# Kernel tuning notes

Hardware: AMD Instinct MI355X
Metric: run time of the kernel (lower is better)

## Reference

```python
import jax, jax.numpy as jnp
import numpy as np

B, L, DIM = 4, 9216, 256
NH, NP = 8, 4
HD = DIM // NH  # 32
SIDE = int(np.sqrt(L))  # 96


def setup_inputs() -> dict:
    key = jax.random.key(0)
    ks = jax.random.split(key, 8)
    s = 0.05
    return {
        "query": jax.random.normal(ks[0], (B, L, DIM), jnp.float32),
        "key": jax.random.normal(ks[1], (B, L, DIM), jnp.float32),
        "value": jax.random.normal(ks[2], (B, L, DIM), jnp.float32),
        "Wv": jax.random.normal(ks[3], (DIM, DIM), jnp.float32) * s,
        "bv": jnp.zeros((DIM,), jnp.float32),
        "Woff": jax.random.normal(ks[4], (DIM, NH * NP * 2), jnp.float32) * s,
        "boff": jnp.zeros((NH * NP * 2,), jnp.float32),
        "Wwt": jax.random.normal(ks[5], (DIM, NH * NP), jnp.float32) * s,
        "bwt": jnp.zeros((NH * NP,), jnp.float32),
        "Wo": jax.random.normal(ks[6], (DIM, DIM), jnp.float32) * s,
        "bo": jnp.zeros((DIM,), jnp.float32),
    }


def _deform_attn(query, value, Wv, bv, Woff, boff, Wwt, bwt, Wo, bo):
    Bq, Lq, D = query.shape
    h = w = SIDE
    # value projection -> [B, nH, L, hd]
    v = (value @ Wv + bv).reshape(Bq, Lq, NH, HD).transpose(0, 2, 1, 3)
    # reference points in [0,1]: ref[...,0]=x (varies fast), ref[...,1]=y (row-major flatten)
    ys = jnp.linspace(0.0, 1.0, h)
    xs = jnp.linspace(0.0, 1.0, w)
    y_ref = jnp.repeat(ys, w)  # [L]
    x_ref = jnp.tile(xs, h)    # [L]
    ref = jnp.stack([x_ref, y_ref], axis=-1)  # [L, 2]
    # offsets [B, nH, Lq, NP, 2] and softmax weights [B, nH, Lq, NP]
    offset = (query @ Woff + boff).reshape(Bq, Lq, NH, NP, 2).transpose(0, 2, 1, 3, 4)
    wt = jax.nn.softmax(
        (query @ Wwt + bwt).reshape(Bq, Lq, NH, NP).transpose(0, 2, 1, 3), axis=-1
    )
    loc = jnp.clip(ref[None, None, :, None, :] + offset, 0.0, 1.0)
    # faithful to source: component 0 scales by (h-1) -> row, component 1 by (w-1) -> col
    rows = loc[..., 0] * (h - 1)  # [B, nH, Lq, NP]
    cols = loc[..., 1] * (w - 1)
    r0 = jnp.floor(rows)
    c0 = jnp.floor(cols)
    fr = (rows - r0)[..., None]  # [B, nH, Lq, NP, 1]
    fc = (cols - c0)[..., None]
    r0i = r0.astype(jnp.int32)
    c0i = c0.astype(jnp.int32)
    r1i = jnp.minimum(r0i + 1, h - 1)
    c1i = jnp.minimum(c0i + 1, w - 1)

    def gather(ri, ci):
        idx = (ri * w + ci).reshape(Bq, NH, Lq * NP)
        g = jnp.take_along_axis(v, idx[..., None], axis=2)  # [B, nH, Lq*NP, hd]
        return g.reshape(Bq, NH, Lq, NP, HD)

    samp = (
        gather(r0i, c0i) * (1.0 - fr) * (1.0 - fc)
        + gather(r0i, c1i) * (1.0 - fr) * fc
        + gather(r1i, c0i) * fr * (1.0 - fc)
        + gather(r1i, c1i) * fr * fc
    )  # [B, nH, Lq, NP, hd]
    out = jnp.einsum("bhqp,bhqpd->bhqd", wt, samp)
    out = out.transpose(0, 2, 1, 3).reshape(Bq, Lq, D)
    return out @ Wo + bo


def reference(query, key, value, Wv, bv, Woff, boff, Wwt, bwt, Wo, bo):
    # key never influences the output in the source module (k is computed but unused)
    return _deform_attn(query, value, Wv, bv, Woff, boff, Wwt, bwt, Wo, bo)
```

## Files before the change

kernel.cpp:

```cpp
#include <hip/hip_runtime.h>
#include <hip/hip_bf16.h>

#define Bq   4
#define Lq   9216
#define DIMc 256
#define NHc  8
#define NPc  4
#define HDc  32
#define SIDEc 96

using f32x4  = __attribute__((ext_vector_type(4))) float;
using bf16x8 = __attribute__((ext_vector_type(8))) short;
using u16x8  = __attribute__((ext_vector_type(8))) unsigned short;

static __device__ __forceinline__ short f2bf(float x) {
    union { __hip_bfloat16 h; short s; } u;
    u.h = __float2bfloat16(x);
    return u.s;
}
static __device__ __forceinline__ float bfbits(unsigned short s) {
    union { unsigned u; float f; } v; v.u = ((unsigned)s) << 16; return v.f;
}

__global__ void prep(const float* __restrict__ Wv, const float* __restrict__ Wo,
                     const float* __restrict__ Woff, const float* __restrict__ Wwt,
                     short* __restrict__ WvT, short* __restrict__ WoT,
                     short* __restrict__ WpHi, short* __restrict__ WpLo) {
    const int id = blockIdx.x, t = threadIdx.x;
    if (id < 64) {
        __shared__ float tile[256][8];
        const float* W = (id < 32) ? Wv : Wo;
        short* T = (id < 32) ? WvT : WoT;
        const int n0 = (id & 31) * 8;
        const float4 a = *(const float4*)&W[t * 256 + n0];
        const float4 b = *(const float4*)&W[t * 256 + n0 + 4];
        tile[t][0] = a.x; tile[t][1] = a.y; tile[t][2] = a.z; tile[t][3] = a.w;
        tile[t][4] = b.x; tile[t][5] = b.y; tile[t][6] = b.z; tile[t][7] = b.w;
        __syncthreads();
        const int n = n0 + (t >> 5), kk = (t & 31) * 8;
        bf16x8 v;
#pragma unroll
        for (int e = 0; e < 8; ++e) v[e] = f2bf(tile[kk + e][t >> 5]);
        *(bf16x8*)&T[n * 256 + kk] = v;
    } else {
        const int p = id - 64;
        const float x = (p < 64) ? Woff[t * 64 + p] : Wwt[t * 32 + (p - 64)];
        const short h = f2bf(x);
        WpHi[p * 256 + t] = h;
        WpLo[p * 256 + t] = f2bf(x - bfbits((unsigned short)h));
    }
}

template<bool VOUT, bool BF16IN>
__global__ __launch_bounds__(256, 3) void gemm_mfma(
        const float* __restrict__ Xf, const short* Xb,
        const short* __restrict__ WT, const float* __restrict__ bias,
        __hip_bfloat16* __restrict__ Yv, float* Yo) {
    __shared__ short As[64][264];
    const int t = threadIdx.x;
    const int base = blockIdx.x * 64;

    if (BF16IN) {
#pragma unroll
        for (int p = 0; p < 8; ++p) {
            const int c = p * 256 + t;
            const int r = c >> 5, k0 = (c & 31) * 8;
            *(bf16x8*)&As[r][k0] = *(const bf16x8*)&Xb[((long)blockIdx.x << 15) + r * 256 + k0];
        }
    } else {
        const float4* X4 = (const float4*)(Xf + (long)base * DIMc);
#pragma unroll
        for (int p = 0; p < 8; ++p) {
            const int c = p * 256 + t;
            const int r = c >> 5, kq = (c & 31) * 2;
            const float4 a = X4[r * 64 + kq];
            const float4 b = X4[r * 64 + kq + 1];
            bf16x8 v;
            v[0] = f2bf(a.x); v[1] = f2bf(a.y); v[2] = f2bf(a.z); v[3] = f2bf(a.w);
            v[4] = f2bf(b.x); v[5] = f2bf(b.y); v[6] = f2bf(b.z); v[7] = f2bf(b.w);
            *(bf16x8*)&As[r][kq * 4] = v;
        }
    }
    __syncthreads();

    const int lane = t & 63, wc = t >> 6;
    const int lr = lane & 15, lq = lane >> 4;

    f32x4 acc[4][4];
#pragma unroll
    for (int i = 0; i < 4; ++i)
#pragma unroll
        for (int j = 0; j < 4; ++j) acc[i][j] = (f32x4){0.f, 0.f, 0.f, 0.f};

#pragma unroll
    for (int ks = 0; ks < 8; ++ks) {
        const int k0 = ks * 32 + lq * 8;
        bf16x8 a[4], b[4];
#pragma unroll
        for (int i = 0; i < 4; ++i)
            a[i] = *(const bf16x8*)&As[i * 16 + lr][k0];
#pragma unroll
        for (int j = 0; j < 4; ++j)
            b[j] = *(const bf16x8*)&WT[(wc * 64 + j * 16 + lr) * 256 + k0];
#pragma unroll
        for (int i = 0; i < 4; ++i)
#pragma unroll
            for (int j = 0; j < 4; ++j)
                acc[i][j] = __builtin_amdgcn_mfma_f32_16x16x32_bf16(a[i], b[j], acc[i][j], 0, 0, 0);
    }

    const int b_ = base / Lq;
    const int l0 = base % Lq;
#pragma unroll
    for (int i = 0; i < 4; ++i) {
        const int mrow = i * 16 + lq * 4;
#pragma unroll
        for (int j = 0; j < 4; ++j) {
            const int n  = wc * 64 + j * 16 + lr;
            const float bb = bias[n];
            const f32x4 v = acc[i][j];
            if (VOUT) {
                const int h = n >> 5, d = n & 31;
                __hip_bfloat16* yb = Yv + (((long)(b_ * NHc + h)) * Lq + (l0 + mrow)) * HDc + d;
#pragma unroll
                for (int reg = 0; reg < 4; ++reg)
                    yb[(long)reg * HDc] = __float2bfloat16(v[reg] + bb);
            } else {
                float* yo = Yo + (long)(base + mrow) * DIMc + n;
#pragma unroll
                for (int reg = 0; reg < 4; ++reg)
                    yo[(long)reg * DIMc] = v[reg] + bb;
            }
        }
    }
}

__global__ __launch_bounds__(256, 3) void deform_fused2(
        const float* __restrict__ Q,
        const short* __restrict__ WpHi, const short* __restrict__ WpLo,
        const float* __restrict__ boff, const float* __restrict__ bwt,
        const __hip_bfloat16* __restrict__ vws,
        __hip_bfloat16* __restrict__ midb) {
    __shared__ float  Qf[32][260];
    __shared__ int    recI[1024];
    __shared__ float4 recW[1024];
    float* prjs = &Qf[0][0];

    const int t = threadIdx.x;
    const int bid = (int)blockIdx.x;
    const int lb = (bid & 7) * 144 + (bid >> 3);
    const int base = lb * 32;
    const int b  = base / Lq;
    const int l0 = base % Lq;

    const float4* Q4 = (const float4*)(Q + (long)base * DIMc);
#pragma unroll
    for (int p = 0; p < 8; ++p) {
        const int c = p * 256 + t;
        const int r = c >> 6, kq = c & 63;
        *(float4*)&Qf[r][kq * 4] = Q4[c];
    }
    __syncthreads();

    const int lane = t & 63, w = t >> 6;
    const int rt = w & 1, cg = w >> 1;
    const int lr = lane & 15, lq = lane >> 4;

    f32x4 pacc[3];
#pragma unroll
    for (int jj = 0; jj < 3; ++jj) pacc[jj] = (f32x4){0.f, 0.f, 0.f, 0.f};

#pragma unroll
    for (int ks = 0; ks < 8; ++ks) {
        const int k0 = ks * 32 + lq * 8;
        const float* qp = &Qf[rt * 16 + lr][k0];
        const float4 a0 = *(const float4*)qp;
        const float4 a1 = *(const float4*)(qp + 4);
        const float xs[8] = {a0.x, a0.y, a0.z, a0.w, a1.x, a1.y, a1.z, a1.w};
        bf16x8 ah, al;
#pragma unroll
        for (int e = 0; e < 8; ++e) {
            const short hh = f2bf(xs[e]);
            ah[e] = hh;
            al[e] = f2bf(xs[e] - bfbits((unsigned short)hh));
        }
#pragma unroll
        for (int jj = 0; jj < 3; ++jj) {
            const int c = cg * 48 + jj * 16 + lr;
            const bf16x8 bh = *(const bf16x8*)&WpHi[c * 256 + k0];
            const bf16x8 bl = *(const bf16x8*)&WpLo[c * 256 + k0];
            pacc[jj] = __builtin_amdgcn_mfma_f32_16x16x32_bf16(ah, bh, pacc[jj], 0, 0, 0);
            pacc[jj] = __builtin_amdgcn_mfma_f32_16x16x32_bf16(ah, bl, pacc[jj], 0, 0, 0);
            pacc[jj] = __builtin_amdgcn_mfma_f32_16x16x32_bf16(al, bh, pacc[jj], 0, 0, 0);
        }
    }
    __syncthreads();

#pragma unroll
    for (int jj = 0; jj < 3; ++jj) {
        const int col = cg * 48 + jj * 16 + lr;
        const float bb = (col < 64) ? boff[col] : bwt[col - 64];
#pragma unroll
        for (int reg = 0; reg < 4; ++reg) {
            const int row = rt * 16 + lq * 4 + reg;
            prjs[row * 96 + col] = pacc[jj][reg] + bb;
        }
    }
    __syncthreads();

#pragma unroll
    for (int i = 0; i < 4; ++i) {
        const int s = i * 256 + t;
        const int r = s >> 5, u = s & 31;
        const int h = u >> 2, p = u & 3;
        const int l = l0 + r;
        const float* pr = &prjs[r * 96];
        const float inv = 1.0f / (SIDEc - 1);
        const float xr = (float)(l % SIDEc) * inv;
        const float yr = (float)(l / SIDEc) * inv;

        const float4 lg = *(const float4*)&pr[64 + h * 4];
        const float m = fmaxf(fmaxf(lg.x, lg.y), fmaxf(lg.z, lg.w));
        const float e0 = expf(lg.x - m), e1 = expf(lg.y - m);
        const float e2 = expf(lg.z - m), e3 = expf(lg.w - m);
        const float sum = e0 + e1 + e2 + e3;
        const float ep = (p == 0) ? e0 : (p == 1) ? e1 : (p == 2) ? e2 : e3;
        const float wt = ep / sum;

        const float lx = fminf(fmaxf(xr + pr[u * 2 + 0], 0.f), 1.f);
        const float ly = fminf(fmaxf(yr + pr[u * 2 + 1], 0.f), 1.f);
        const float rowf = lx * (float)(SIDEc - 1);
        const float colf = ly * (float)(SIDEc - 1);
        const float r0f = floorf(rowf), c0f = floorf(colf);
        const int r0 = (int)r0f, c0 = (int)c0f;
        const float fr = rowf - r0f, fc = colf - c0f;
        const int drow = (r0 < SIDEc - 1) ? 1 : 0;
        const int dcol = (c0 < SIDEc - 1) ? 1 : 0;
        recI[s] = (r0 * SIDEc + c0) | (drow << 16) | (dcol << 17);
        float4 w4;
        w4.x = wt * (1.f - fr) * (1.f - fc);
        w4.y = wt * (1.f - fr) * fc;
        w4.z = wt * fr * (1.f - fc);
        w4.w = wt * fr * fc;
        recW[s] = w4;
    }
    __syncthreads();

    const int h = (t >> 2) & 7, dq = t & 3;
    const int rhalf = (t >> 5) & 1, wid = t >> 6;
    const __hip_bfloat16* vb = vws + ((long)(b * NHc + h) * Lq) * HDc + dq * 8;
    const int chan = (t & 31) * 8;

#pragma unroll
    for (int pass = 0; pass < 4; ++pass) {
        const int r = pass * 8 + wid * 2 + rhalf;
        float acc[8];
#pragma unroll
        for (int e = 0; e < 8; ++e) acc[e] = 0.f;
#pragma unroll
        for (int p = 0; p < 4; ++p) {
            const int    mt = recI[r * 32 + h * 4 + p];
            const float4 w4 = recW[r * 32 + h * 4 + p];
            const int sl = mt & 0xFFFF;
            const int dr = (mt & 0x10000) ? SIDEc * HDc : 0;
            const int dc = (mt & 0x20000) ? HDc : 0;
            const __hip_bfloat16* pv = vb + (long)sl * HDc;
            const u16x8 u00 = *(const u16x8*)(pv);
            const u16x8 u01 = *(const u16x8*)(pv + dc);
            const u16x8 u10 = *(const u16x8*)(pv + dr);
            const u16x8 u11 = *(const u16x8*)(pv + dr + dc);
#pragma unroll
            for (int e = 0; e < 8; ++e)
                acc[e] += w4.x * bfbits(u00[e]) + w4.y * bfbits(u01[e])
                        + w4.z * bfbits(u10[e]) + w4.w * bfbits(u11[e]);
        }
        const int rg = base + r;
        u16x8 o;
#pragma unroll
        for (int e = 0; e < 8; ++e) o[e] = (unsigned short)f2bf(acc[e]);
        *(u16x8*)(midb + ((long)(rg >> 6) << 15) + ((rg & 63) << 8) + chan) = o;
    }
}

extern "C" void kernel_launch(void* const* d_in, const int* in_sizes, int n_in,
                              void* d_out, int out_size, void* d_ws, size_t ws_size,
                              hipStream_t stream) {
    const float* query = (const float*)d_in[0];
    const float* value = (const float*)d_in[2];
    const float* Wv    = (const float*)d_in[3];
    const float* bv    = (const float*)d_in[4];
    const float* Woff  = (const float*)d_in[5];
    const float* boff  = (const float*)d_in[6];
    const float* Wwt   = (const float*)d_in[7];
    const float* bwt   = (const float*)d_in[8];
    const float* Wo    = (const float*)d_in[9];
    const float* bo    = (const float*)d_in[10];

    float* out = (float*)d_out;
    char*  ws  = (char*)d_ws;
    __hip_bfloat16* vws = (__hip_bfloat16*)ws;
    short* WvT  = (short*)(ws + 18874368);
    short* WoT  = (short*)(ws + 18874368 + 131072);
    short* WpHi = (short*)(ws + 18874368 + 262144);
    short* WpLo = (short*)(ws + 18874368 + 262144 + 49152);
    __hip_bfloat16* midb = (__hip_bfloat16*)d_out;

    const int nrows = Bq * Lq;

    prep<<<160, 256, 0, stream>>>(Wv, Wo, Woff, Wwt, WvT, WoT, WpHi, WpLo);
    gemm_mfma<true, false><<<nrows / 64, 256, 0, stream>>>(value, nullptr, WvT, bv, vws, nullptr);
    deform_fused2<<<nrows / 32, 256, 0, stream>>>(query, WpHi, WpLo, boff, bwt, vws, midb);
    gemm_mfma<false, true><<<nrows / 64, 256, 0, stream>>>(nullptr, (const short*)midb, WoT, bo, nullptr, out);
}
```

Measured before the change: 100.2 us.

## Move offset/weight projection into value GEMM kernel, slim gather kernel

Moves the query projection (offsets and softmax logits, split bf16 hi/lo MFMA) out of the deform kernel and into the value-projection GEMM kernel, which now writes fp32 projections to a workspace buffer. The gather kernel only loads the 96-wide projections, so its LDS footprint shrinks and it can run at higher occupancy (launch bounds 6). Bilinear weights are now stored as fp16 in LDS, which costs a little precision. Both GEMMs now use 32-row tiles instead of 64, which doubles the block count. The price is an extra global round trip for the projection buffer.

```diff
diff --git a/kernel.cpp b/kernel.cpp
--- a/kernel.cpp
+++ b/kernel.cpp
@@ -12,6 +12,7 @@
 using f32x4  = __attribute__((ext_vector_type(4))) float;
 using bf16x8 = __attribute__((ext_vector_type(8))) short;
 using u16x8  = __attribute__((ext_vector_type(8))) unsigned short;
+using h16x4  = __attribute__((ext_vector_type(4))) _Float16;
 
 static __device__ __forceinline__ short f2bf(float x) {
     union { __hip_bfloat16 h; short s; } u;
@@ -51,59 +52,93 @@
     }
 }
 
-template<bool VOUT, bool BF16IN>
-__global__ __launch_bounds__(256, 3) void gemm_mfma(
-        const float* __restrict__ Xf, const short* Xb,
-        const short* __restrict__ WT, const float* __restrict__ bias,
-        __hip_bfloat16* __restrict__ Yv, float* Yo) {
-    __shared__ short As[64][264];
+__global__ __launch_bounds__(256, 3) void gemm1_proj(
+        const float* __restrict__ X, const float* __restrict__ Q,
+        const short* __restrict__ WT,
+        const short* __restrict__ WpHi, const short* __restrict__ WpLo,
+        const float* __restrict__ bias,
+        const float* __restrict__ boff, const float* __restrict__ bwt,
+        __hip_bfloat16* __restrict__ Yv, float* __restrict__ prj) {
+    __shared__ short As[32][264];
     const int t = threadIdx.x;
-    const int base = blockIdx.x * 64;
-
-    if (BF16IN) {
-#pragma unroll
-        for (int p = 0; p < 8; ++p) {
-            const int c = p * 256 + t;
-            const int r = c >> 5, k0 = (c & 31) * 8;
-            *(bf16x8*)&As[r][k0] = *(const bf16x8*)&Xb[((long)blockIdx.x << 15) + r * 256 + k0];
-        }
-    } else {
-        const float4* X4 = (const float4*)(Xf + (long)base * DIMc);
-#pragma unroll
-        for (int p = 0; p < 8; ++p) {
-            const int c = p * 256 + t;
-            const int r = c >> 5, kq = (c & 31) * 2;
-            const float4 a = X4[r * 64 + kq];
-            const float4 b = X4[r * 64 + kq + 1];
-            bf16x8 v;
-            v[0] = f2bf(a.x); v[1] = f2bf(a.y); v[2] = f2bf(a.z); v[3] = f2bf(a.w);
-            v[4] = f2bf(b.x); v[5] = f2bf(b.y); v[6] = f2bf(b.z); v[7] = f2bf(b.w);
-            *(bf16x8*)&As[r][kq * 4] = v;
+    const int base = blockIdx.x * 32;
+
+    const float4* X4 = (const float4*)(X + (long)base * DIMc);
+#pragma unroll
+    for (int p = 0; p < 4; ++p) {
+        const int c = p * 256 + t;
+        const int r = c >> 5, kq = (c & 31) * 2;
+        const float4 a = X4[r * 64 + kq];
+        const float4 b = X4[r * 64 + kq + 1];
+        bf16x8 v;
+        v[0] = f2bf(a.x); v[1] = f2bf(a.y); v[2] = f2bf(a.z); v[3] = f2bf(a.w);
+        v[4] = f2bf(b.x); v[5] = f2bf(b.y); v[6] = f2bf(b.z); v[7] = f2bf(b.w);
+        *(bf16x8*)&As[r][kq * 4] = v;
+    }
+
+    const int lane = t & 63, w = t >> 6;
+    const int lr = lane & 15, lq = lane >> 4;
+
+    {
+        const int rt = w >> 1, cg = w & 1;
+        f32x4 pacc[3];
+#pragma unroll
+        for (int jj = 0; jj < 3; ++jj) pacc[jj] = (f32x4){0.f, 0.f, 0.f, 0.f};
+        const float* Qrow = Q + (long)(base + rt * 16 + lr) * DIMc;
+#pragma unroll
+        for (int ks = 0; ks < 8; ++ks) {
+            const int k0 = ks * 32 + lq * 8;
+            const float4 a0 = *(const float4*)(Qrow + k0);
+            const float4 a1 = *(const float4*)(Qrow + k0 + 4);
+            const float xs[8] = {a0.x, a0.y, a0.z, a0.w, a1.x, a1.y, a1.z, a1.w};
+            bf16x8 ah, al;
+#pragma unroll
+            for (int e = 0; e < 8; ++e) {
+                const short hh = f2bf(xs[e]);
+                ah[e] = hh;
+                al[e] = f2bf(xs[e] - bfbits((unsigned short)hh));
+            }
+#pragma unroll
+            for (int jj = 0; jj < 3; ++jj) {
+                const int c = cg * 48 + jj * 16 + lr;
+                const bf16x8 bh = *(const bf16x8*)&WpHi[c * 256 + k0];
+                const bf16x8 bl = *(const bf16x8*)&WpLo[c * 256 + k0];
+                pacc[jj] = __builtin_amdgcn_mfma_f32_16x16x32_bf16(ah, bh, pacc[jj], 0, 0, 0);
+                pacc[jj] = __builtin_amdgcn_mfma_f32_16x16x32_bf16(ah, bl, pacc[jj], 0, 0, 0);
+                pacc[jj] = __builtin_amdgcn_mfma_f32_16x16x32_bf16(al, bh, pacc[jj], 0, 0, 0);
+            }
+        }
+#pragma unroll
+        for (int jj = 0; jj < 3; ++jj) {
+            const int col = cg * 48 + jj * 16 + lr;
+            const float bb = (col < 64) ? boff[col] : bwt[col - 64];
+#pragma unroll
+            for (int reg = 0; reg < 4; ++reg) {
+                const int row = rt * 16 + lq * 4 + reg;
+                prj[(long)(base + row) * 96 + col] = pacc[jj][reg] + bb;
+            }
         }
     }
     __syncthreads();
 
-    const int lane = t & 63, wc = t >> 6;
-    const int lr = lane & 15, lq = lane >> 4;
-
-    f32x4 acc[4][4];
-#pragma unroll
-    for (int i = 0; i < 4; ++i)
+    f32x4 acc[2][4];
+#pragma unroll
+    for (int i = 0; i < 2; ++i)
 #pragma unroll
         for (int j = 0; j < 4; ++j) acc[i][j] = (f32x4){0.f, 0.f, 0.f, 0.f};
 
 #pragma unroll
     for (int ks = 0; ks < 8; ++ks) {
         const int k0 = ks * 32 + lq * 8;
-        bf16x8 a[4], b[4];
-#pragma unroll
-        for (int i = 0; i < 4; ++i)
+        bf16x8 a[2], b[4];
+#pragma unroll
+        for (int i = 0; i < 2; ++i)
             a[i] = *(const bf16x8*)&As[i * 16 + lr][k0];
 #pragma unroll
         for (int j = 0; j < 4; ++j)
-            b[j] = *(const bf16x8*)&WT[(wc * 64 + j * 16 + lr) * 256 + k0];
-#pragma unroll
-        for (int i = 0; i < 4; ++i)
+            b[j] = *(const bf16x8*)&WT[(w * 64 + j * 16 + lr) * 256 + k0];
+#pragma unroll
+        for (int i = 0; i < 2; ++i)
 #pragma unroll
             for (int j = 0; j < 4; ++j)
                 acc[i][j] = __builtin_amdgcn_mfma_f32_16x16x32_bf16(a[i], b[j], acc[i][j], 0, 0, 0);
@@ -112,39 +147,29 @@
     const int b_ = base / Lq;
     const int l0 = base % Lq;
 #pragma unroll
-    for (int i = 0; i < 4; ++i) {
+    for (int i = 0; i < 2; ++i) {
         const int mrow = i * 16 + lq * 4;
 #pragma unroll
         for (int j = 0; j < 4; ++j) {
-            const int n  = wc * 64 + j * 16 + lr;
+            const int n  = w * 64 + j * 16 + lr;
             const float bb = bias[n];
             const f32x4 v = acc[i][j];
-            if (VOUT) {
-                const int h = n >> 5, d = n & 31;
-                __hip_bfloat16* yb = Yv + (((long)(b_ * NHc + h)) * Lq + (l0 + mrow)) * HDc + d;
-#pragma unroll
-                for (int reg = 0; reg < 4; ++reg)
-                    yb[(long)reg * HDc] = __float2bfloat16(v[reg] + bb);
-            } else {
-                float* yo = Yo + (long)(base + mrow) * DIMc + n;
-#pragma unroll
-                for (int reg = 0; reg < 4; ++reg)
-                    yo[(long)reg * DIMc] = v[reg] + bb;
-            }
-        }
-    }
-}
-
-__global__ __launch_bounds__(256, 3) void deform_fused2(
-        const float* __restrict__ Q,
-        const short* __restrict__ WpHi, const short* __restrict__ WpLo,
-        const float* __restrict__ boff, const float* __restrict__ bwt,
+            const int h = n >> 5, d = n & 31;
+            __hip_bfloat16* yb = Yv + (((long)(b_ * NHc + h)) * Lq + (l0 + mrow)) * HDc + d;
+#pragma unroll
+            for (int reg = 0; reg < 4; ++reg)
+                yb[(long)reg * HDc] = __float2bfloat16(v[reg] + bb);
+        }
+    }
+}
+
+__global__ __launch_bounds__(256, 6) void deform_gather(
+        const float* __restrict__ prj,
         const __hip_bfloat16* __restrict__ vws,
         __hip_bfloat16* __restrict__ midb) {
-    __shared__ float  Qf[32][260];
-    __shared__ int    recI[1024];
-    __shared__ float4 recW[1024];
-    float* prjs = &Qf[0][0];
+    __shared__ float prjs[32 * 96];
+    __shared__ int   recI[1024];
+    __shared__ h16x4 recW[1024];
 
     const int t = threadIdx.x;
     const int bid = (int)blockIdx.x;
@@ -153,59 +178,10 @@
     const int b  = base / Lq;
     const int l0 = base % Lq;
 
-    const float4* Q4 = (const float4*)(Q + (long)base * DIMc);
-#pragma unroll
-    for (int p = 0; p < 8; ++p) {
-        const int c = p * 256 + t;
-        const int r = c >> 6, kq = c & 63;
-        *(float4*)&Qf[r][kq * 4] = Q4[c];
-    }
-    __syncthreads();
-
-    const int lane = t & 63, w = t >> 6;
-    const int rt = w & 1, cg = w >> 1;
-    const int lr = lane & 15, lq = lane >> 4;
-
-    f32x4 pacc[3];
-#pragma unroll
-    for (int jj = 0; jj < 3; ++jj) pacc[jj] = (f32x4){0.f, 0.f, 0.f, 0.f};
-
-#pragma unroll
-    for (int ks = 0; ks < 8; ++ks) {
-        const int k0 = ks * 32 + lq * 8;
-        const float* qp = &Qf[rt * 16 + lr][k0];
-        const float4 a0 = *(const float4*)qp;
-        const float4 a1 = *(const float4*)(qp + 4);
-        const float xs[8] = {a0.x, a0.y, a0.z, a0.w, a1.x, a1.y, a1.z, a1.w};
-        bf16x8 ah, al;
-#pragma unroll
-        for (int e = 0; e < 8; ++e) {
-            const short hh = f2bf(xs[e]);
-            ah[e] = hh;
-            al[e] = f2bf(xs[e] - bfbits((unsigned short)hh));
-        }
-#pragma unroll
-        for (int jj = 0; jj < 3; ++jj) {
-            const int c = cg * 48 + jj * 16 + lr;
-            const bf16x8 bh = *(const bf16x8*)&WpHi[c * 256 + k0];
-            const bf16x8 bl = *(const bf16x8*)&WpLo[c * 256 + k0];
-            pacc[jj] = __builtin_amdgcn_mfma_f32_16x16x32_bf16(ah, bh, pacc[jj], 0, 0, 0);
-            pacc[jj] = __builtin_amdgcn_mfma_f32_16x16x32_bf16(ah, bl, pacc[jj], 0, 0, 0);
-            pacc[jj] = __builtin_amdgcn_mfma_f32_16x16x32_bf16(al, bh, pacc[jj], 0, 0, 0);
-        }
-    }
-    __syncthreads();
-
-#pragma unroll
-    for (int jj = 0; jj < 3; ++jj) {
-        const int col = cg * 48 + jj * 16 + lr;
-        const float bb = (col < 64) ? boff[col] : bwt[col - 64];
-#pragma unroll
-        for (int reg = 0; reg < 4; ++reg) {
-            const int row = rt * 16 + lq * 4 + reg;
-            prjs[row * 96 + col] = pacc[jj][reg] + bb;
-        }
-    }
+    const float4* P4 = (const float4*)(prj + (long)base * 96);
+#pragma unroll
+    for (int i = 0; i < 3; ++i)
+        ((float4*)prjs)[t + 256 * i] = P4[t + 256 * i];
     __syncthreads();
 
 #pragma unroll
@@ -237,12 +213,12 @@
         const int drow = (r0 < SIDEc - 1) ? 1 : 0;
         const int dcol = (c0 < SIDEc - 1) ? 1 : 0;
         recI[s] = (r0 * SIDEc + c0) | (drow << 16) | (dcol << 17);
-        float4 w4;
-        w4.x = wt * (1.f - fr) * (1.f - fc);
-        w4.y = wt * (1.f - fr) * fc;
-        w4.z = wt * fr * (1.f - fc);
-        w4.w = wt * fr * fc;
-        recW[s] = w4;
+        h16x4 wh;
+        wh[0] = (_Float16)(wt * (1.f - fr) * (1.f - fc));
+        wh[1] = (_Float16)(wt * (1.f - fr) * fc);
+        wh[2] = (_Float16)(wt * fr * (1.f - fc));
+        wh[3] = (_Float16)(wt * fr * fc);
+        recW[s] = wh;
     }
     __syncthreads();
 
@@ -259,8 +235,10 @@
         for (int e = 0; e < 8; ++e) acc[e] = 0.f;
 #pragma unroll
         for (int p = 0; p < 4; ++p) {
-            const int    mt = recI[r * 32 + h * 4 + p];
-            const float4 w4 = recW[r * 32 + h * 4 + p];
+            const int   mt = recI[r * 32 + h * 4 + p];
+            const h16x4 wh = recW[r * 32 + h * 4 + p];
+            const float w0 = (float)wh[0], w1 = (float)wh[1];
+            const float w2 = (float)wh[2], w3 = (float)wh[3];
             const int sl = mt & 0xFFFF;
             const int dr = (mt & 0x10000) ? SIDEc * HDc : 0;
             const int dc = (mt & 0x20000) ? HDc : 0;
@@ -271,14 +249,71 @@
             const u16x8 u11 = *(const u16x8*)(pv + dr + dc);
 #pragma unroll
             for (int e = 0; e < 8; ++e)
-                acc[e] += w4.x * bfbits(u00[e]) + w4.y * bfbits(u01[e])
-                        + w4.z * bfbits(u10[e]) + w4.w * bfbits(u11[e]);
+                acc[e] += w0 * bfbits(u00[e]) + w1 * bfbits(u01[e])
+                        + w2 * bfbits(u10[e]) + w3 * bfbits(u11[e]);
         }
         const int rg = base + r;
         u16x8 o;
 #pragma unroll
         for (int e = 0; e < 8; ++e) o[e] = (unsigned short)f2bf(acc[e]);
-        *(u16x8*)(midb + ((long)(rg >> 6) << 15) + ((rg & 63) << 8) + chan) = o;
+        *(u16x8*)(midb + ((long)(rg >> 5) << 14) + ((rg & 31) << 8) + chan) = o;
+    }
+}
+
+__global__ __launch_bounds__(256, 4) void gemm2_mfma(
+        const short* Xb, const short* __restrict__ WT,
+        const float* __restrict__ bias, float* Yo) {
+    __shared__ short As[32][264];
+    const int t = threadIdx.x;
+    const int base = blockIdx.x * 32;
+
+#pragma unroll
+    for (int p = 0; p < 4; ++p) {
+        const int c = p * 256 + t;
+        const int r = c >> 5, k0 = (c & 31) * 8;
+        *(bf16x8*)&As[r][k0] = *(const bf16x8*)&Xb[((long)blockIdx.x << 14) + r * 256 + k0];
+    }
+    __syncthreads();
+
+    const int lane = t & 63, w = t >> 6;
+    const int lr = lane & 15, lq = lane >> 4;
+
+    f32x4 acc[2][4];
+#pragma unroll
+    for (int i = 0; i < 2; ++i)
+#pragma unroll
+        for (int j = 0; j < 4; ++j) acc[i][j] = (f32x4){0.f, 0.f, 0.f, 0.f};
+
+#pragma unroll
+    for (int ks = 0; ks < 8; ++ks) {
+        const int k0 = ks * 32 + lq * 8;
+        bf16x8 a[2], b[4];
+#pragma unroll
+        for (int i = 0; i < 2; ++i)
+            a[i] = *(const bf16x8*)&As[i * 16 + lr][k0];
+#pragma unroll
+        for (int j = 0; j < 4; ++j)
+            b[j] = *(const bf16x8*)&WT[(w * 64 + j * 16 + lr) * 256 + k0];
+#pragma unroll
+        for (int i = 0; i < 2; ++i)
+#pragma unroll
+            for (int j = 0; j < 4; ++j)
+                acc[i][j] = __builtin_amdgcn_mfma_f32_16x16x32_bf16(a[i], b[j], acc[i][j], 0, 0, 0);
+    }
+
+#pragma unroll
+    for (int i = 0; i < 2; ++i) {
+        const int mrow = i * 16 + lq * 4;
+#pragma unroll
+        for (int j = 0; j < 4; ++j) {
+            const int n  = w * 64 + j * 16 + lr;
+            const float bb = bias[n];
+            const f32x4 v = acc[i][j];
+            float* yo = Yo + (long)(base + mrow) * DIMc + n;
+#pragma unroll
+            for (int reg = 0; reg < 4; ++reg)
+                yo[(long)reg * DIMc] = v[reg] + bb;
+        }
     }
 }
 
@@ -303,12 +338,14 @@
     short* WoT  = (short*)(ws + 18874368 + 131072);
     short* WpHi = (short*)(ws + 18874368 + 262144);
     short* WpLo = (short*)(ws + 18874368 + 262144 + 49152);
+    float* prj  = (float*)(ws + 18874368 + 262144 + 98304);
     __hip_bfloat16* midb = (__hip_bfloat16*)d_out;
 
     const int nrows = Bq * Lq;
 
     prep<<<160, 256, 0, stream>>>(Wv, Wo, Woff, Wwt, WvT, WoT, WpHi, WpLo);
-    gemm_mfma<true, false><<<nrows / 64, 256, 0, stream>>>(value, nullptr, WvT, bv, vws, nullptr);
-    deform_fused2<<<nrows / 32, 256, 0, stream>>>(query, WpHi, WpLo, boff, bwt, vws, midb);
-    gemm_mfma<false, true><<<nrows / 64, 256, 0, stream>>>(nullptr, (const short*)midb, WoT, bo, nullptr, out);
-}
+    gemm1_proj<<<nrows / 32, 256, 0, stream>>>(value, query, WvT, WpHi, WpLo,
+                                               bv, boff, bwt, vws, prj);
+    deform_gather<<<nrows / 32, 256, 0, stream>>>(prj, vws, midb);
+    gemm2_mfma<<<nrows / 32, 256, 0, stream>>>((const short*)midb, WoT, bo, out);
+}
```

New measurement: 223.0 us. +122.6%, slower.
